# Optimization experiments

Hardware: AMD Instinct MI355X
Metric: run time of the kernel (lower is better)

## Reference

```python
import jax, jax.numpy as jnp
import numpy as np

DIM = 192
HEADS = 6
WS = 7          # window size
SHIFT = 3       # shift size
HID = 768       # mlp hidden
EPS = 1e-5


def _rel_pos_index(ws):
    coords = np.stack(np.meshgrid(np.arange(ws), np.arange(ws), indexing='ij'))  # (2, ws, ws)
    cf = coords.reshape(2, -1)                       # (2, ws*ws)
    rel = cf[:, :, None] - cf[:, None, :]            # (2, N, N)
    rel = rel.transpose(1, 2, 0).astype(np.int64)
    rel[:, :, 0] += ws - 1
    rel[:, :, 1] += ws - 1
    rel[:, :, 0] *= 2 * ws - 1
    return jnp.asarray(rel.sum(-1))                  # (N, N)

REL_IDX = _rel_pos_index(WS)


def _layernorm(x, w, b):
    mu = jnp.mean(x, axis=-1, keepdims=True)
    var = jnp.mean(jnp.square(x - mu), axis=-1, keepdims=True)
    return (x - mu) * jax.lax.rsqrt(var + EPS) * w + b


def setup_inputs() -> dict:
    key = jax.random.key(0)
    ks = jax.random.split(key, 8)
    B, H, W = 32, 56, 56
    s = 0.02
    return {
        'x': jax.random.normal(ks[0], (B, H * W, DIM), jnp.float32),
        'norm1_w': jnp.ones((DIM,), jnp.float32),
        'norm1_b': jnp.zeros((DIM,), jnp.float32),
        'qkv_w': jax.random.normal(ks[1], (3 * DIM, DIM), jnp.float32) * s,
        'qkv_b': jnp.zeros((3 * DIM,), jnp.float32),
        'rpb_table': jax.random.normal(ks[2], ((2 * WS - 1) ** 2, HEADS), jnp.float32) * s,
        'proj_w': jax.random.normal(ks[3], (DIM, DIM), jnp.float32) * s,
        'proj_b': jnp.zeros((DIM,), jnp.float32),
        'norm2_w': jnp.ones((DIM,), jnp.float32),
        'norm2_b': jnp.zeros((DIM,), jnp.float32),
        'fc1_w': jax.random.normal(ks[4], (HID, DIM), jnp.float32) * s,
        'fc1_b': jnp.zeros((HID,), jnp.float32),
        'fc2_w': jax.random.normal(ks[5], (DIM, HID), jnp.float32) * s,
        'fc2_b': jnp.zeros((DIM,), jnp.float32),
        'H': H,
        'W': W,
    }


def reference(x, norm1_w, norm1_b, qkv_w, qkv_b, rpb_table, proj_w, proj_b,
              norm2_w, norm2_b, fc1_w, fc1_b, fc2_w, fc2_b, H, W):
    B, L, C = x.shape
    d = C // HEADS
    scale = d ** -0.5
    N = WS * WS

    shortcut = x
    h = _layernorm(x, norm1_w, norm1_b).reshape(B, H, W, C)
    if SHIFT > 0:
        h = jnp.roll(h, shift=(-SHIFT, -SHIFT), axis=(1, 2))

    # window partition -> (B * nW, N, C)
    h = h.reshape(B, H // WS, WS, W // WS, WS, C).transpose(0, 1, 3, 2, 4, 5)
    hw = h.reshape(-1, N, C)

    # windowed attention (NOTE: the torch block never passes a shift mask)
    qkv = hw @ qkv_w.T + qkv_b                                    # (B_, N, 3C)
    qkv = qkv.reshape(-1, N, 3, HEADS, d).transpose(2, 0, 3, 1, 4)
    q, k, v = qkv[0] * scale, qkv[1], qkv[2]                      # (B_, h, N, d)
    attn = jnp.einsum('bhnd,bhmd->bhnm', q, k)
    bias = rpb_table[REL_IDX].transpose(2, 0, 1)                  # (h, N, N)
    attn = jax.nn.softmax(attn + bias[None], axis=-1)
    out = jnp.einsum('bhnm,bhmd->bhnd', attn, v)
    out = out.transpose(0, 2, 1, 3).reshape(-1, N, C)
    out = out @ proj_w.T + proj_b

    # window reverse -> (B, H, W, C)
    out = out.reshape(B, H // WS, W // WS, WS, WS, C).transpose(0, 1, 3, 2, 4, 5)
    out = out.reshape(B, H, W, C)
    if SHIFT > 0:
        out = jnp.roll(out, shift=(SHIFT, SHIFT), axis=(1, 2))

    x = shortcut + out.reshape(B, L, C)
    h2 = _layernorm(x, norm2_w, norm2_b)
    mlp = jax.nn.gelu(h2 @ fc1_w.T + fc1_b, approximate=False) @ fc2_w.T + fc2_b
    return x + mlp
```

## Files before the change

kernel.cpp:

```cpp
#include <hip/hip_runtime.h>
#include <hip/hip_bf16.h>
#include <cmath>

typedef float f32x4 __attribute__((ext_vector_type(4)));
typedef __bf16 bf16x8 __attribute__((ext_vector_type(8)));
typedef __bf16 bf16x4 __attribute__((ext_vector_type(4)));

#define WS_SZ 7
#define SHIFT 3
#define HGRID 56
#define C_DIM 192
#define NHEADS 6
#define HDIM 32
#define NTOK 100352
#define NWIN 2048

__device__ __forceinline__ int win_to_tok(int wrow) {
    int w = wrow / 49, i = wrow - w * 49;
    int b = w >> 6, rem = w & 63;
    int wy = rem >> 3, wx = rem & 7;
    int yi = i / 7, xi = i - yi * 7;
    int y = wy * 7 + yi + SHIFT; if (y >= HGRID) y -= HGRID;
    int x = wx * 7 + xi + SHIFT; if (x >= HGRID) x -= HGRID;
    return b * (HGRID * HGRID) + y * HGRID + x;
}

__global__ __launch_bounds__(256)
void cvt_all_kernel(const float* __restrict__ qkvw, const float* __restrict__ projw,
                    const float* __restrict__ fc1w, const float* __restrict__ fc2w,
                    __bf16* __restrict__ qkvw_b, __bf16* __restrict__ projw_b,
                    __bf16* __restrict__ fc1w_b, __bf16* __restrict__ fc2w_b)
{
    int idx = blockIdx.x * 256 + threadIdx.x;
    if (idx >= 55296) return;
    const float* src; __bf16* dst; int off;
    if (idx < 13824)      { src = qkvw;  dst = qkvw_b;  off = idx; }
    else if (idx < 18432) { src = projw; dst = projw_b; off = idx - 13824; }
    else if (idx < 36864) { src = fc1w;  dst = fc1w_b;  off = idx - 18432; }
    else                  { src = fc2w;  dst = fc2w_b;  off = idx - 36864; }
    float4 a = ((const float4*)src)[off * 2];
    float4 b = ((const float4*)src)[off * 2 + 1];
    bf16x8 o;
    o[0] = (__bf16)a.x; o[1] = (__bf16)a.y; o[2] = (__bf16)a.z; o[3] = (__bf16)a.w;
    o[4] = (__bf16)b.x; o[5] = (__bf16)b.y; o[6] = (__bf16)b.z; o[7] = (__bf16)b.w;
    ((bf16x8*)dst)[off] = o;
}

__global__ __launch_bounds__(256)
void bias_expand_kernel(const float* __restrict__ rpb, float* __restrict__ bias_p)
{
    int idx = blockIdx.x * 256 + threadIdx.x;
    if (idx >= NHEADS * 64 * 64) return;
    int h = idx >> 12, rem = idx & 4095;
    int i = rem >> 6, j = rem & 63;
    float v = -1e30f;
    if (i < 49 && j < 49) {
        int yi = i / 7, xi = i - yi * 7;
        int yj = j / 7, xj = j - yj * 7;
        int ri = (yi - yj + 6) * 13 + (xi - xj + 6);
        v = rpb[ri * NHEADS + h];
    }
    bias_p[idx] = v;
}

template<int WINDOWED>
__global__ __launch_bounds__(256)
void ln_kernel(const float* __restrict__ x, const float* __restrict__ w,
               const float* __restrict__ b, __bf16* __restrict__ out)
{
    int r = blockIdx.x * 4 + (threadIdx.x >> 6);
    int lane = threadIdx.x & 63;
    int src = WINDOWED ? win_to_tok(r) : r;
    const float* xp = x + (size_t)src * C_DIM;
    float v0 = xp[lane], v1 = xp[lane + 64], v2 = xp[lane + 128];
    float s = v0 + v1 + v2;
    float sq = v0 * v0 + v1 * v1 + v2 * v2;
    #pragma unroll
    for (int off = 32; off; off >>= 1) {
        s  += __shfl_xor(s, off);
        sq += __shfl_xor(sq, off);
    }
    float mu = s * (1.f / C_DIM);
    float rs = rsqrtf(sq * (1.f / C_DIM) - mu * mu + 1e-5f);
    __bf16* op = out + (size_t)r * C_DIM;
    op[lane]       = (__bf16)((v0 - mu) * rs * w[lane]       + b[lane]);
    op[lane + 64]  = (__bf16)((v1 - mu) * rs * w[lane + 64]  + b[lane + 64]);
    op[lane + 128] = (__bf16)((v2 - mu) * rs * w[lane + 128] + b[lane + 128]);
}

__global__ __launch_bounds__(256, 3)
void qkv_gemm_kernel(const __bf16* __restrict__ A, const __bf16* __restrict__ W,
                     const float* __restrict__ bias, __bf16* __restrict__ outp)
{
    __shared__ __bf16 As[128 * 40];
    __shared__ __bf16 Bs[192 * 40];
    const int tid = threadIdx.x;
    const int wave = tid >> 6, lane = tid & 63;
    const int wm = wave >> 1, wn = wave & 1;
    const int l15 = lane & 15, q4 = lane >> 4, q8 = q4 << 3;
    const int m0 = blockIdx.y * 128, n0 = blockIdx.x * 192;

    f32x4 acc[4][6];
    f32x4 zero = {0.f, 0.f, 0.f, 0.f};
    #pragma unroll
    for (int i = 0; i < 4; i++)
        #pragma unroll
        for (int j = 0; j < 6; j++) acc[i][j] = zero;

    for (int kt = 0; kt < 192; kt += 32) {
        __syncthreads();
        #pragma unroll
        for (int it = 0; it < 2; it++) {
            int idx = it * 256 + tid;
            int r = idx >> 2, c = (idx & 3) << 3;
            *(uint4*)(&As[r * 40 + c]) =
                *(const uint4*)(A + (size_t)(m0 + r) * 192 + kt + c);
        }
        #pragma unroll
        for (int it = 0; it < 3; it++) {
            int idx = it * 256 + tid;
            int r = idx >> 2, c = (idx & 3) << 3;
            *(uint4*)(&Bs[r * 40 + c]) =
                *(const uint4*)(W + (size_t)(n0 + r) * 192 + kt + c);
        }
        __syncthreads();
        bf16x8 af[4], bfr[6];
        #pragma unroll
        for (int fm = 0; fm < 4; fm++)
            af[fm] = *(const bf16x8*)(&As[(wm * 64 + fm * 16 + l15) * 40 + q8]);
        #pragma unroll
        for (int fn = 0; fn < 6; fn++)
            bfr[fn] = *(const bf16x8*)(&Bs[(wn * 96 + fn * 16 + l15) * 40 + q8]);
        #pragma unroll
        for (int fm = 0; fm < 4; fm++)
            #pragma unroll
            for (int fn = 0; fn < 6; fn++)
                acc[fm][fn] = __builtin_amdgcn_mfma_f32_16x16x32_bf16(
                    af[fm], bfr[fn], acc[fm][fn], 0, 0, 0);
    }

    #pragma unroll
    for (int fm = 0; fm < 4; fm++) {
        #pragma unroll
        for (int fn = 0; fn < 6; fn++) {
            int c = n0 + wn * 96 + fn * 16 + l15;
            float bv = bias[c];
            #pragma unroll
            for (int r = 0; r < 4; r++) {
                int m = m0 + wm * 64 + fm * 16 + q4 * 4 + r;
                outp[(size_t)m * 576 + c] = (__bf16)(acc[fm][fn][r] + bv);
            }
        }
    }
}

__global__ __launch_bounds__(256, 3)
void proj_ln_kernel(const __bf16* __restrict__ A,
                    const __bf16* __restrict__ W,
                    const float* __restrict__ pb,
                    const float* __restrict__ x,
                    const float* __restrict__ n2w, const float* __restrict__ n2b,
                    float* __restrict__ out,
                    __bf16* __restrict__ lnout)
{
    __shared__ __align__(16) __bf16 As[64 * 200];
    __shared__ __bf16 Bs[192 * 40];
    const int tid = threadIdx.x;
    const int wn = tid >> 6, lane = tid & 63;
    const int l15 = lane & 15, q4 = lane >> 4, q8 = q4 << 3;
    const int m0 = blockIdx.x * 64;

    float bvp[12];
    #pragma unroll
    for (int tn = 0; tn < 12; ++tn) bvp[tn] = pb[tn * 16 + l15];

    #pragma unroll
    for (int it = 0; it < 6; ++it) {
        int idx = it * 256 + tid;
        int r = idx / 24, c = (idx - r * 24) << 3;
        *(uint4*)(&As[r * 200 + c]) =
            *(const uint4*)(A + (size_t)(m0 + r) * 192 + c);
    }

    f32x4 zero = {0.f, 0.f, 0.f, 0.f};
    f32x4 acc[12];
    #pragma unroll
    for (int tn = 0; tn < 12; ++tn) acc[tn] = zero;

    for (int kt = 0; kt < 6; ++kt) {
        __syncthreads();
        #pragma unroll
        for (int it = 0; it < 3; ++it) {
            int idx = it * 256 + tid;
            int rr = idx >> 2, cc = (idx & 3) << 3;
            *(uint4*)(&Bs[rr * 40 + cc]) =
                *(const uint4*)(W + (size_t)rr * 192 + kt * 32 + cc);
        }
        __syncthreads();
        bf16x8 af = *(const bf16x8*)(&As[(wn * 16 + l15) * 200 + kt * 32 + q8]);
        #pragma unroll
        for (int tn = 0; tn < 12; ++tn) {
            bf16x8 bfr = *(const bf16x8*)(&Bs[(tn * 16 + l15) * 40 + q8]);
            acc[tn] = __builtin_amdgcn_mfma_f32_16x16x32_bf16(af, bfr, acc[tn], 0, 0, 0);
        }
    }

    float* Cs = (float*)As;
    const int rowt = tid >> 3, lane8 = tid & 7;
    const int c0 = lane8 * 24;
    #pragma unroll
    for (int pass = 0; pass < 2; ++pass) {
        __syncthreads();
        if ((wn >> 1) == pass) {
            int rl0 = (wn & 1) * 16 + q4 * 4;
            #pragma unroll
            for (int tn = 0; tn < 12; ++tn) {
                int c = tn * 16 + l15;
                #pragma unroll
                for (int r = 0; r < 4; ++r)
                    Cs[(rl0 + r) * 196 + c] = acc[tn][r] + bvp[tn];
            }
        }
        __syncthreads();
        int m = m0 + pass * 32 + rowt;
        int t = win_to_tok(m);
        const float* xp = x + (size_t)t * C_DIM + c0;
        float* op = out + (size_t)t * C_DIM + c0;
        float v[24];
        float s = 0.f, sq = 0.f;
        #pragma unroll
        for (int e = 0; e < 24; ++e) {
            float o = xp[e] + Cs[rowt * 196 + c0 + e];
            v[e] = o;
            s += o; sq += o * o;
        }
        #pragma unroll
        for (int e4 = 0; e4 < 6; ++e4) {
            float4 g = { v[e4*4], v[e4*4+1], v[e4*4+2], v[e4*4+3] };
            *(float4*)(op + e4 * 4) = g;
        }
        s  += __shfl_xor(s, 1);  s  += __shfl_xor(s, 2);  s  += __shfl_xor(s, 4);
        sq += __shfl_xor(sq, 1); sq += __shfl_xor(sq, 2); sq += __shfl_xor(sq, 4);
        float mu = s * (1.f / C_DIM);
        float rs = rsqrtf(sq * (1.f / C_DIM) - mu * mu + 1e-5f);
        __bf16* lp = lnout + (size_t)t * C_DIM + c0;
        #pragma unroll
        for (int e8 = 0; e8 < 3; ++e8) {
            bf16x8 ob;
            #pragma unroll
            for (int e = 0; e < 8; ++e) {
                int c = c0 + e8 * 8 + e;
                ob[e] = (__bf16)((v[e8*8+e] - mu) * rs * n2w[c] + n2b[c]);
            }
            *(bf16x8*)(lp + e8 * 8) = ob;
        }
    }
}

__global__ __launch_bounds__(256, 3)
void mlp_fused_kernel(const __bf16* __restrict__ lnA,
                      const __bf16* __restrict__ w1,
                      const float* __restrict__ b1,
                      const __bf16* __restrict__ w2,
                      const float* __restrict__ b2,
                      float* __restrict__ out)
{
    __shared__ __align__(16) __bf16 As[64 * 200];
    __shared__ __bf16 Hs[64 * 72];
    const int tid = threadIdx.x;
    const int wn = tid >> 6, lane = tid & 63;
    const int l15 = lane & 15, q4 = lane >> 4, q8 = q4 << 3;
    const int m0 = blockIdx.x * 64;

    const __bf16* w1base = w1 + (size_t)(wn * 16 + l15) * 192 + q8;
    const __bf16* w2base = w2 + (size_t)(wn * 48 + l15) * 768 + q8;

    f32x4 zero = {0.f, 0.f, 0.f, 0.f};

    bf16x8 w1f[2][6];
    #pragma unroll
    for (int kt = 0; kt < 6; ++kt)
        w1f[0][kt] = *(const bf16x8*)(w1base + kt * 32);

    float bv1s[12];
    #pragma unroll
    for (int ch = 0; ch < 12; ++ch)
        bv1s[ch] = b1[ch * 64 + wn * 16 + l15];
    float bv2s[3];
    #pragma unroll
    for (int tn = 0; tn < 3; ++tn)
        bv2s[tn] = b2[wn * 48 + tn * 16 + l15];

    #pragma unroll
    for (int it = 0; it < 6; ++it) {
        int idx = it * 256 + tid;
        int r = idx / 24, c = (idx - r * 24) << 3;
        *(uint4*)(&As[r * 200 + c]) =
            *(const uint4*)(lnA + (size_t)(m0 + r) * 192 + c);
    }
    __syncthreads();

    f32x4 acc2[4][3];
    #pragma unroll
    for (int tm = 0; tm < 4; ++tm)
        #pragma unroll
        for (int tn = 0; tn < 3; ++tn) acc2[tm][tn] = zero;

    bf16x8 w2f[6];

    #pragma unroll
    for (int ch = 0; ch < 12; ++ch) {
        const int h0 = ch * 64;
        const int cur = ch & 1, nxt = cur ^ 1;

        if (ch < 11) {
            #pragma unroll
            for (int kt = 0; kt < 6; ++kt)
                w1f[nxt][kt] = *(const bf16x8*)(w1base + (size_t)(h0 + 64) * 192 + kt * 32);
        }
        #pragma unroll
        for (int ks = 0; ks < 2; ++ks)
            #pragma unroll
            for (int tn = 0; tn < 3; ++tn)
                w2f[ks * 3 + tn] = *(const bf16x8*)(w2base + (size_t)(tn * 16) * 768 + h0 + ks * 32);

        f32x4 acc1[4];
        #pragma unroll
        for (int tm = 0; tm < 4; ++tm) acc1[tm] = zero;
        #pragma unroll
        for (int kt = 0; kt < 6; ++kt)
            #pragma unroll
            for (int tm = 0; tm < 4; ++tm) {
                bf16x8 af = *(const bf16x8*)(&As[(tm * 16 + l15) * 200 + kt * 32 + q8]);
                acc1[tm] = __builtin_amdgcn_mfma_f32_16x16x32_bf16(
                    af, w1f[cur][kt], acc1[tm], 0, 0, 0);
            }

        __syncthreads();

        {
            const float bv = bv1s[ch];
            #pragma unroll
            for (int tm = 0; tm < 4; ++tm)
                #pragma unroll
                for (int r = 0; r < 4; ++r) {
                    int row = tm * 16 + q4 * 4 + r;
                    float v = acc1[tm][r] + bv;
                    float g = v * __builtin_amdgcn_rcpf(1.f + __expf(-1.702f * v));
                    Hs[row * 72 + wn * 16 + l15] = (__bf16)g;
                }
        }
        __syncthreads();

        #pragma unroll
        for (int ks = 0; ks < 2; ++ks)
            #pragma unroll
            for (int tm = 0; tm < 4; ++tm) {
                bf16x8 ap = *(const bf16x8*)(&Hs[(tm * 16 + l15) * 72 + ks * 32 + q8]);
                #pragma unroll
                for (int tn = 0; tn < 3; ++tn)
                    acc2[tm][tn] = __builtin_amdgcn_mfma_f32_16x16x32_bf16(
                        ap, w2f[ks * 3 + tn], acc2[tm][tn], 0, 0, 0);
            }
    }

    float* Cs = (float*)As;
    #pragma unroll
    for (int pass = 0; pass < 2; ++pass) {
        if (pass) __syncthreads();
        #pragma unroll
        for (int tmh = 0; tmh < 2; ++tmh) {
            int tm = pass * 2 + tmh;
            #pragma unroll
            for (int tn = 0; tn < 3; ++tn) {
                int c = wn * 48 + tn * 16 + l15;
                float bv = bv2s[tn];
                #pragma unroll
                for (int r = 0; r < 4; ++r) {
                    int rl = tmh * 16 + q4 * 4 + r;
                    Cs[rl * 196 + c] = acc2[tm][tn][r] + bv;
                }
            }
        }
        __syncthreads();
        #pragma unroll
        for (int it = 0; it < 6; ++it) {
            int f = it * 256 + tid;
            int row = f / 48, c4 = f - row * 48;
            float4* gp = (float4*)(out + (size_t)(m0 + pass * 32 + row) * C_DIM) + c4;
            float4 g = *gp;
            const float* lp = &Cs[row * 196 + c4 * 4];
            g.x += lp[0]; g.y += lp[1]; g.z += lp[2]; g.w += lp[3];
            *gp = g;
        }
    }
}

__global__ __launch_bounds__(64)
void attn_mfma_kernel(const __bf16* __restrict__ qkv,
                      const float* __restrict__ bias_p,
                      __bf16* __restrict__ out)
{
    const int lane = threadIdx.x & 63;
    const int pair = blockIdx.x;
    const int w = pair / 6, head = pair - (pair / 6) * 6;

    __shared__ __bf16 vsT[32 * 72];
    __shared__ __bf16 Ps[64 * 72];

    const int l15 = lane & 15, q4 = lane >> 4, q8 = q4 << 3;
    const size_t qbase = (size_t)w * 49 * 576 + head * 32;

    bf16x8 qf[4], kf[4];
    #pragma unroll
    for (int t = 0; t < 4; ++t) {
        int row = t * 16 + l15;
        int rq = row < 49 ? row : 48;
        qf[t] = *(const bf16x8*)(qkv + qbase + (size_t)rq * 576 + q8);
        kf[t] = *(const bf16x8*)(qkv + qbase + (size_t)rq * 576 + 192 + q8);
    }

    {
        int j0 = lane >> 2, dq = (lane & 3) << 3;
        #pragma unroll
        for (int p = 0; p < 4; ++p) {
            int j = p * 16 + j0;
            if (j < 49) {
                bf16x8 vv = *(const bf16x8*)(qkv + qbase + (size_t)j * 576 + 384 + dq);
                #pragma unroll
                for (int e = 0; e < 8; ++e)
                    vsT[(dq + e) * 72 + j] = vv[e];
            }
        }
        for (int idx = lane; idx < 32 * 15; idx += 64) {
            int dd = idx / 15, jj = 49 + (idx - dd * 15);
            vsT[dd * 72 + jj] = (__bf16)0.f;
        }
    }

    f32x4 sc[4][4];
    f32x4 zero = {0.f, 0.f, 0.f, 0.f};
    #pragma unroll
    for (int tn = 0; tn < 4; ++tn)
        #pragma unroll
        for (int tm = 0; tm < 4; ++tm) sc[tn][tm] = zero;
    __builtin_amdgcn_s_setprio(1);
    #pragma unroll
    for (int tn = 0; tn < 4; ++tn)
        #pragma unroll
        for (int tm = 0; tm < 4; ++tm)
            sc[tn][tm] = __builtin_amdgcn_mfma_f32_16x16x32_bf16(
                kf[tn], qf[tm], sc[tn][tm], 0, 0, 0);
    __builtin_amdgcn_s_setprio(0);

    const float scale = 0.17677669529663687f;
    const float* bb = bias_p + head * 4096;
    const int jb4 = q4 * 4;
    #pragma unroll
    for (int tm = 0; tm < 4; ++tm) {
        int i = tm * 16 + l15;
        float4 bp[4];
        #pragma unroll
        for (int tn = 0; tn < 4; ++tn)
            bp[tn] = *(const float4*)(bb + i * 64 + tn * 16 + jb4);
        float v[4][4];
        #pragma unroll
        for (int tn = 0; tn < 4; ++tn) {
            v[tn][0] = sc[tn][tm][0] * scale + bp[tn].x;
            v[tn][1] = sc[tn][tm][1] * scale + bp[tn].y;
            v[tn][2] = sc[tn][tm][2] * scale + bp[tn].z;
            v[tn][3] = sc[tn][tm][3] * scale + bp[tn].w;
        }
        float mx = v[0][0];
        #pragma unroll
        for (int tn = 0; tn < 4; ++tn)
            #pragma unroll
            for (int r = 0; r < 4; ++r) mx = fmaxf(mx, v[tn][r]);
        mx = fmaxf(mx, __shfl_xor(mx, 16));
        mx = fmaxf(mx, __shfl_xor(mx, 32));
        float sm = 0.f;
        #pragma unroll
        for (int tn = 0; tn < 4; ++tn)
            #pragma unroll
            for (int r = 0; r < 4; ++r) {
                float e = __expf(v[tn][r] - mx);
                v[tn][r] = e;
                sm += e;
            }
        sm += __shfl_xor(sm, 16);
        sm += __shfl_xor(sm, 32);
        float inv = __builtin_amdgcn_rcpf(sm);
        if (i < 49) {
            #pragma unroll
            for (int tn = 0; tn < 4; ++tn) {
                int jb = tn * 16 + jb4;
                bf16x4 pk;
                #pragma unroll
                for (int r = 0; r < 4; ++r)
                    pk[r] = (__bf16)(v[tn][r] * inv);
                *(bf16x4*)(&Ps[i * 72 + jb]) = pk;
            }
        }
    }


    f32x4 oc[4][2];
    #pragma unroll
    for (int tm = 0; tm < 4; ++tm)
        #pragma unroll
        for (int tn = 0; tn < 2; ++tn) oc[tm][tn] = zero;
    #pragma unroll
    for (int ks = 0; ks < 2; ++ks) {
        bf16x8 bv[2];
        #pragma unroll
        for (int tn = 0; tn < 2; ++tn)
            bv[tn] = *(const bf16x8*)(vsT + (tn * 16 + l15) * 72 + ks * 32 + q8);
        __builtin_amdgcn_s_setprio(1);
        #pragma unroll
        for (int tm = 0; tm < 4; ++tm) {
            bf16x8 ap = *(const bf16x8*)(Ps + (tm * 16 + l15) * 72 + ks * 32 + q8);
            #pragma unroll
            for (int tn = 0; tn < 2; ++tn)
                oc[tm][tn] = __builtin_amdgcn_mfma_f32_16x16x32_bf16(
                    ap, bv[tn], oc[tm][tn], 0, 0, 0);
        }
        __builtin_amdgcn_s_setprio(0);
    }

    #pragma unroll
    for (int tm = 0; tm < 4; ++tm) {
        #pragma unroll
        for (int r = 0; r < 4; ++r) {
            int m = tm * 16 + q4 * 4 + r;
            if (m < 49) {
                __bf16* op = out + (size_t)(w * 49 + m) * C_DIM + head * 32;
                #pragma unroll
                for (int tn = 0; tn < 2; ++tn)
                    op[tn * 16 + l15] = (__bf16)(oc[tm][tn][r]);
            }
        }
    }
}

extern "C" void kernel_launch(void* const* d_in, const int* in_sizes, int n_in,
                              void* d_out, int out_size, void* d_ws, size_t ws_size,
                              hipStream_t stream) {
    const float* x     = (const float*)d_in[0];
    const float* n1w   = (const float*)d_in[1];
    const float* n1b   = (const float*)d_in[2];
    const float* qkvw  = (const float*)d_in[3];
    const float* qkvb  = (const float*)d_in[4];
    const float* rpb   = (const float*)d_in[5];
    const float* projw = (const float*)d_in[6];
    const float* projb = (const float*)d_in[7];
    const float* n2w   = (const float*)d_in[8];
    const float* n2b   = (const float*)d_in[9];
    const float* fc1w  = (const float*)d_in[10];
    const float* fc1b  = (const float*)d_in[11];
    const float* fc2w  = (const float*)d_in[12];
    const float* fc2b  = (const float*)d_in[13];
    float* out = (float*)d_out;
    char* ws = (char*)d_ws;

    __bf16* bufA    = (__bf16*)ws;
    __bf16* bufQ    = (__bf16*)(ws + 38535168);
    __bf16* lnout   = bufQ;
    __bf16* qkvw_b  = (__bf16*)(ws + 154140672);
    __bf16* projw_b = (__bf16*)(ws + 154361856);
    __bf16* fc1w_b  = (__bf16*)(ws + 154435584);
    __bf16* fc2w_b  = (__bf16*)(ws + 154730496);
    float*  bias_p  = (float*) (ws + 155025408);

    cvt_all_kernel<<<216, 256, 0, stream>>>(qkvw, projw, fc1w, fc2w,
                                            qkvw_b, projw_b, fc1w_b, fc2w_b);
    bias_expand_kernel<<<(NHEADS*64*64 + 255)/256, 256, 0, stream>>>(rpb, bias_p);

    ln_kernel<1><<<NTOK / 4, 256, 0, stream>>>(x, n1w, n1b, bufA);
    qkv_gemm_kernel<<<dim3(3, NTOK / 128), 256, 0, stream>>>(
        bufA, qkvw_b, qkvb, bufQ);
    attn_mfma_kernel<<<NWIN * NHEADS, 64, 0, stream>>>(bufQ, bias_p, bufA);
    proj_ln_kernel<<<NTOK / 64, 256, 0, stream>>>(
        bufA, projw_b, projb, x, n2w, n2b, out, lnout);
    mlp_fused_kernel<<<NTOK / 64, 256, 0, stream>>>(
        lnout, fc1w_b, fc1b, fc2w_b, fc2b, out);
}
```

Before: 469.9 us.

## Store QKV in per-window per-head contiguous slabs and narrow GEMM N tile

```diff
diff --git a/kernel.cpp b/kernel.cpp
--- a/kernel.cpp
+++ b/kernel.cpp
@@ -14,6 +14,9 @@
 #define HDIM 32
 #define NTOK 100352
 #define NWIN 2048
+#define QSLAB 1568
+#define QWH   (3 * QSLAB)
+#define QWIN  (NHEADS * QWH)
 
 __device__ __forceinline__ int win_to_tok(int wrow) {
     int w = wrow / 49, i = wrow - w * 49;
@@ -88,25 +91,26 @@
     op[lane + 128] = (__bf16)((v2 - mu) * rs * w[lane + 128] + b[lane + 128]);
 }
 
-__global__ __launch_bounds__(256, 3)
+__global__ __launch_bounds__(256)
 void qkv_gemm_kernel(const __bf16* __restrict__ A, const __bf16* __restrict__ W,
                      const float* __restrict__ bias, __bf16* __restrict__ outp)
 {
     __shared__ __bf16 As[128 * 40];
-    __shared__ __bf16 Bs[192 * 40];
+    __shared__ __bf16 Bs[64 * 40];
     const int tid = threadIdx.x;
     const int wave = tid >> 6, lane = tid & 63;
     const int wm = wave >> 1, wn = wave & 1;
     const int l15 = lane & 15, q4 = lane >> 4, q8 = q4 << 3;
-    const int m0 = blockIdx.y * 128, n0 = blockIdx.x * 192;
-
-    f32x4 acc[4][6];
+    const int m0 = blockIdx.y * 128, n0 = blockIdx.x * 64;
+
+    f32x4 acc[4][2];
     f32x4 zero = {0.f, 0.f, 0.f, 0.f};
     #pragma unroll
     for (int i = 0; i < 4; i++)
         #pragma unroll
-        for (int j = 0; j < 6; j++) acc[i][j] = zero;
-
+        for (int j = 0; j < 2; j++) acc[i][j] = zero;
+
+    const int br = tid >> 2, bc = (tid & 3) << 3;
     for (int kt = 0; kt < 192; kt += 32) {
         __syncthreads();
         #pragma unroll
@@ -116,39 +120,39 @@
             *(uint4*)(&As[r * 40 + c]) =
                 *(const uint4*)(A + (size_t)(m0 + r) * 192 + kt + c);
         }
-        #pragma unroll
-        for (int it = 0; it < 3; it++) {
-            int idx = it * 256 + tid;
-            int r = idx >> 2, c = (idx & 3) << 3;
-            *(uint4*)(&Bs[r * 40 + c]) =
-                *(const uint4*)(W + (size_t)(n0 + r) * 192 + kt + c);
-        }
-        __syncthreads();
-        bf16x8 af[4], bfr[6];
+        *(uint4*)(&Bs[br * 40 + bc]) =
+            *(const uint4*)(W + (size_t)(n0 + br) * 192 + kt + bc);
+        __syncthreads();
+        bf16x8 af[4], bfr[2];
         #pragma unroll
         for (int fm = 0; fm < 4; fm++)
             af[fm] = *(const bf16x8*)(&As[(wm * 64 + fm * 16 + l15) * 40 + q8]);
         #pragma unroll
-        for (int fn = 0; fn < 6; fn++)
-            bfr[fn] = *(const bf16x8*)(&Bs[(wn * 96 + fn * 16 + l15) * 40 + q8]);
+        for (int fn = 0; fn < 2; fn++)
+            bfr[fn] = *(const bf16x8*)(&Bs[(wn * 32 + fn * 16 + l15) * 40 + q8]);
         #pragma unroll
         for (int fm = 0; fm < 4; fm++)
             #pragma unroll
-            for (int fn = 0; fn < 6; fn++)
+            for (int fn = 0; fn < 2; fn++)
                 acc[fm][fn] = __builtin_amdgcn_mfma_f32_16x16x32_bf16(
                     af[fm], bfr[fn], acc[fm][fn], 0, 0, 0);
     }
 
     #pragma unroll
-    for (int fm = 0; fm < 4; fm++) {
-        #pragma unroll
-        for (int fn = 0; fn < 6; fn++) {
-            int c = n0 + wn * 96 + fn * 16 + l15;
-            float bv = bias[c];
+    for (int fn = 0; fn < 2; fn++) {
+        int cb = n0 + wn * 32 + fn * 16;
+        int s = cb / 192, hc = cb - s * 192;
+        int h = hc >> 5, jb = hc & 31;
+        size_t hs_off = (size_t)(h * 3 + s) * QSLAB + jb + l15;
+        float bv = bias[cb + l15];
+        #pragma unroll
+        for (int fm = 0; fm < 4; fm++) {
             #pragma unroll
             for (int r = 0; r < 4; r++) {
                 int m = m0 + wm * 64 + fm * 16 + q4 * 4 + r;
-                outp[(size_t)m * 576 + c] = (__bf16)(acc[fm][fn][r] + bv);
+                int w = m / 49, i = m - w * 49;
+                outp[(size_t)w * QWIN + hs_off + i * 32] =
+                    (__bf16)(acc[fm][fn][r] + bv);
             }
         }
     }
@@ -409,15 +413,15 @@
     __shared__ __bf16 Ps[64 * 72];
 
     const int l15 = lane & 15, q4 = lane >> 4, q8 = q4 << 3;
-    const size_t qbase = (size_t)w * 49 * 576 + head * 32;
+    const __bf16* base = qkv + (size_t)(w * NHEADS + head) * QWH;
 
     bf16x8 qf[4], kf[4];
     #pragma unroll
     for (int t = 0; t < 4; ++t) {
         int row = t * 16 + l15;
         int rq = row < 49 ? row : 48;
-        qf[t] = *(const bf16x8*)(qkv + qbase + (size_t)rq * 576 + q8);
-        kf[t] = *(const bf16x8*)(qkv + qbase + (size_t)rq * 576 + 192 + q8);
+        qf[t] = *(const bf16x8*)(base + rq * 32 + q8);
+        kf[t] = *(const bf16x8*)(base + QSLAB + rq * 32 + q8);
     }
 
     {
@@ -426,7 +430,7 @@
         for (int p = 0; p < 4; ++p) {
             int j = p * 16 + j0;
             if (j < 49) {
-                bf16x8 vv = *(const bf16x8*)(qkv + qbase + (size_t)j * 576 + 384 + dq);
+                bf16x8 vv = *(const bf16x8*)(base + 2 * QSLAB + j * 32 + dq);
                 #pragma unroll
                 for (int e = 0; e < 8; ++e)
                     vsT[(dq + e) * 72 + j] = vv[e];
@@ -576,7 +580,7 @@
     bias_expand_kernel<<<(NHEADS*64*64 + 255)/256, 256, 0, stream>>>(rpb, bias_p);
 
     ln_kernel<1><<<NTOK / 4, 256, 0, stream>>>(x, n1w, n1b, bufA);
-    qkv_gemm_kernel<<<dim3(3, NTOK / 128), 256, 0, stream>>>(
+    qkv_gemm_kernel<<<dim3(9, NTOK / 128), 256, 0, stream>>>(
         bufA, qkvw_b, qkvb, bufQ);
     attn_mfma_kernel<<<NWIN * NHEADS, 64, 0, stream>>>(bufQ, bias_p, bufA);
     proj_ln_kernel<<<NTOK / 64, 256, 0, stream>>>(
```

Result: no change. 468.5 us (-0.3%).
